# Optimization experiments

Measured on AMD Instinct MI355X. Metric: run time of the kernel, lower is better.

The kernel has to match this reference:

```python
import jax, jax.numpy as jnp
import numpy as np

B, C, D, H, W, K = 2, 192, 48, 48, 48, 7
EPS_LN = 1e-6
EPS_GRN = 1e-6


def setup_inputs() -> dict:
    key = jax.random.key(0)
    ks = jax.random.split(key, 8)
    sc = 0.02
    return {
        "x": jax.random.normal(ks[0], (B, C, D, H, W), jnp.float32),
        # depthwise conv kernel in DHWIO layout: [K,K,K,1,C] (torch weight [C,1,K,K,K])
        "conv_w": jax.random.normal(ks[1], (K, K, K, 1, C), jnp.float32) * sc,
        "conv_b": jnp.zeros((C,), jnp.float32),
        "ln_g": jnp.ones((C,), jnp.float32),
        "ln_b": jnp.zeros((C,), jnp.float32),
        "w1": jax.random.normal(ks[2], (C, 4 * C), jnp.float32) * sc,
        "b1": jnp.zeros((4 * C,), jnp.float32),
        "grn_gamma": jax.random.normal(ks[3], (4 * C,), jnp.float32) * sc,
        "grn_beta": jax.random.normal(ks[4], (4 * C,), jnp.float32) * sc,
        "w2": jax.random.normal(ks[5], (4 * C, C), jnp.float32) * sc,
        "b2": jnp.zeros((C,), jnp.float32),
    }


def reference(x, conv_w, conv_b, ln_g, ln_b, w1, b1, grn_gamma, grn_beta, w2, b2):
    c = x.shape[1]
    # NCDHW -> NDHWC (channels-last, as Permute([0,2,3,4,1]) after the conv)
    xc = jnp.transpose(x, (0, 2, 3, 4, 1))
    # depthwise conv3d, kernel 7, pad 3 (SAME for stride 1)
    y = jax.lax.conv_general_dilated(
        xc, conv_w, window_strides=(1, 1, 1), padding="SAME",
        dimension_numbers=("NDHWC", "DHWIO", "NDHWC"),
        feature_group_count=c,
    ) + conv_b
    # LayerNorm over channel dim, eps=1e-6 (biased variance, like torch)
    mu = jnp.mean(y, axis=-1, keepdims=True)
    var = jnp.mean(jnp.square(y - mu), axis=-1, keepdims=True)
    y = (y - mu) * jax.lax.rsqrt(var + EPS_LN) * ln_g + ln_b
    # MLP up + exact GELU
    y = jax.nn.gelu(y @ w1 + b1, approximate=False)
    # GRN: global L2 over spatial dims per channel
    gx = jnp.sqrt(jnp.sum(y * y, axis=(1, 2, 3), keepdims=True))  # [B,1,1,1,4C]
    nx = gx / (jnp.mean(gx, axis=-1, keepdims=True) + EPS_GRN)
    y = grn_gamma * (y * nx) + grn_beta + y
    # MLP down, permute back, residual
    y = y @ w2 + b2
    return jnp.transpose(y, (0, 4, 1, 2, 3)) + x
```

## Files before the change

kernel.cpp:

```cpp
#include <hip/hip_runtime.h>
#include <math.h>

#define Bn 2
#define Cn 192
#define Dn 48
#define Hn 48
#define Wn 48
#define C4 768
#define DHW (Dn*Hn*Wn)
#define CDHW ((long)Cn*DHW)

typedef __attribute__((ext_vector_type(8))) short bf16x8;
typedef __attribute__((ext_vector_type(4))) float f32x4;

__device__ inline float bf2f(unsigned short u) {
    union { float f; unsigned int i; } v; v.i = ((unsigned int)u) << 16; return v.f;
}
__device__ inline unsigned short f2bf(float f) {
    union { float f; unsigned int i; } v; v.f = f;
    unsigned int r = v.i + 0x7FFFu + ((v.i >> 16) & 1u);
    return (unsigned short)(r >> 16);
}
__device__ inline float blo(unsigned int u) {
    union { unsigned int i; float f; } v; v.i = u << 16; return v.f;
}
__device__ inline float bhi(unsigned int u) {
    union { unsigned int i; float f; } v; v.i = u & 0xffff0000u; return v.f;
}
__device__ inline unsigned int cvtpk_bf16(float lo, float hi) {
    unsigned int r;
    asm("v_cvt_pk_bf16_f32 %0, %1, %2" : "=v"(r) : "v"(lo), "v"(hi));
    return r;
}

__global__ __launch_bounds__(256)
void btoep_k(const float* __restrict__ cw, unsigned short* __restrict__ btp)
{
    int idx = blockIdx.x * 256 + threadIdx.x;
    int lane = idx & 63;
    int t = idx >> 6;
    int kdkh = t % 49, c = t / 49;
    int n = lane & 15, g = lane >> 4;
    unsigned short v[8];
#pragma unroll
    for (int j = 0; j < 8; ++j) {
        int kw = 8 * g + j - n;
        v[j] = (kw >= 0 && kw <= 6) ? f2bf(cw[(kdkh * 7 + kw) * Cn + c])
                                    : (unsigned short)0;
    }
    *(uint4*)(btp + (size_t)idx * 8) = *(uint4*)v;
}

#define TD 8
#define TH 16
#define TW 16
#define HD (TD+6)
#define HH (TH+6)

__global__ __launch_bounds__(128)
void conv_dw(const float* __restrict__ x, const unsigned short* __restrict__ btp,
             const float* __restrict__ cb, unsigned short* __restrict__ yc)
{
    __shared__ unsigned int xt[HD * HH * 16];
    int c = blockIdx.y;
    int s = blockIdx.x;
    int wt = s % 3, ht = (s / 3) % 3, dt = s / 9;
    int d0 = dt * TD, h0 = ht * TH, w0 = wt * TW;
    int tid = threadIdx.x;

    const float* xb = x + (long)c * DHW;
    for (int u = tid; u < HD * HH * 16; u += 128) {
        int pr = u & 15, row = u >> 4;
        int hh2 = row % HH, dd = row / HH;
        int gd = d0 - 3 + dd, gh = h0 - 3 + hh2;
        int gw0 = w0 - 3 + pr * 2;
        bool okp = (unsigned)gd < 48u && (unsigned)gh < 48u;
        const float* xr = xb + (gd * 48 + gh) * 48;
        float v0 = (okp && (unsigned)gw0 < 48u) ? xr[gw0] : 0.0f;
        float v1 = (okp && (unsigned)(gw0 + 1) < 48u) ? xr[gw0 + 1] : 0.0f;
        xt[(row << 4) + ((((pr >> 2) ^ (row & 3)) << 2) | (pr & 3))] = cvtpk_bf16(v0, v1);
    }
    __syncthreads();

    int lane = tid & 63, wv = tid >> 6;
    int lr = lane & 15, g = lane >> 4;
    float bias = cb[c];
    f32x4 acc[4];
#pragma unroll
    for (int t = 0; t < 4; ++t) acc[t] = (f32x4){bias, bias, bias, bias};

    const unsigned short* bchan = btp + (size_t)c * 49 * 512;
    const unsigned short* xt16 = (const unsigned short*)xt;

    for (int kh = 0; kh < 7; ++kh) {
        bf16x8 Bf[7];
#pragma unroll
        for (int kd = 0; kd < 7; ++kd)
            Bf[kd] = *(const bf16x8*)(bchan + (size_t)((kd * 7 + kh) * 64 + lane) * 8);
        bf16x8 Af[10];
#pragma unroll
        for (int p = 0; p < 10; ++p) {
            int r = (4 * wv + p) * HH + kh + lr;
            Af[p] = *(const bf16x8*)(xt16 + (r << 5) + ((g ^ (r & 3)) << 3));
        }
#pragma unroll
        for (int kd = 0; kd < 7; ++kd)
#pragma unroll
            for (int t = 0; t < 4; ++t)
                acc[t] = __builtin_amdgcn_mfma_f32_16x16x32_bf16(
                    Af[kd + t], Bf[kd], acc[t], 0, 0, 0);
    }

    unsigned short* yb = yc + (long)c * DHW;
#pragma unroll
    for (int t = 0; t < 4; ++t) {
        int d = d0 + 4 * wv + t;
#pragma unroll
        for (int i = 0; i < 4; ++i) {
            int h = h0 + g * 4 + i;
            yb[((long)d * 48 + h) * 48 + w0 + lr] = f2bf(acc[t][i]);
        }
    }
}

__global__ __launch_bounds__(256)
void ln_kernel(const unsigned short* __restrict__ yc, const float* __restrict__ g,
               const float* __restrict__ lb, unsigned short* __restrict__ y1)
{
    __shared__ float tile[Cn * Wn];
    __shared__ float qs1[4][48], qs2[4][48];
    __shared__ float mu_s[Wn], rs_s[Wn];
    int dh = blockIdx.x;
    long rowbase = (long)dh * Wn;
    for (int l = threadIdx.x; l < Cn * 24; l += 256) {
        int c = l / 24, wp = l % 24;
        unsigned int u = *(const unsigned int*)&yc[rowbase + (long)c * DHW + wp * 2];
        tile[c * Wn + wp * 2]     = blo(u);
        tile[c * Wn + wp * 2 + 1] = bhi(u);
    }
    __syncthreads();
    if (threadIdx.x < 192) {
        int w = threadIdx.x >> 2, q = threadIdx.x & 3;
        float s1 = 0.f, s2 = 0.f;
        for (int cc = 0; cc < 48; ++cc) {
            float v = tile[(cc * 4 + q) * Wn + w];
            s1 += v; s2 = fmaf(v, v, s2);
        }
        qs1[q][w] = s1; qs2[q][w] = s2;
    }
    __syncthreads();
    if (threadIdx.x < 48) {
        int w = threadIdx.x;
        float s1 = qs1[0][w] + qs1[1][w] + qs1[2][w] + qs1[3][w];
        float s2 = qs2[0][w] + qs2[1][w] + qs2[2][w] + qs2[3][w];
        float mu = s1 * (1.0f / Cn);
        float var = s2 * (1.0f / Cn) - mu * mu;
        mu_s[w] = mu;
        rs_s[w] = rsqrtf(var + 1e-6f);
    }
    __syncthreads();
    long obase = (long)dh * Wn * Cn;
    for (int l = threadIdx.x; l < Cn * Wn; l += 256) {
        int w = l / Cn, c = l % Cn;
        float val = (tile[c * Wn + w] - mu_s[w]) * rs_s[w] * g[c] + lb[c];
        y1[obase + l] = f2bf(val);
    }
}

__global__ __launch_bounds__(256)
void wtrans(const float* __restrict__ W, unsigned short* __restrict__ Wt, int K, int N)
{
    int idx = blockIdx.x * 256 + threadIdx.x;
    if (idx >= K * N) return;
    int n = idx / K, k = idx % K;
    Wt[idx] = f2bf(W[(long)k * N + n]);
}

__global__ __launch_bounds__(256)
void wscale(const float* __restrict__ W2, const float* __restrict__ gx2,
            const float* __restrict__ gamma, unsigned short* __restrict__ W2s)
{
    __shared__ float red[256];
    int t = threadIdx.x;
    float s = 0.f;
#pragma unroll
    for (int i = 0; i < 3; ++i) s += sqrtf(gx2[t + i * 256]);
    red[t] = s; __syncthreads();
    for (int st = 128; st > 0; st >>= 1) {
        if (t < st) red[t] += red[t + st];
        __syncthreads();
    }
    float inv = 1.0f / (red[0] * (1.0f / C4) + 1e-6f);
    int idx = blockIdx.x * 256 + t;
    int n = idx / C4, k = idx % C4;
    float snx = 1.0f + gamma[k] * sqrtf(gx2[k]) * inv;
    W2s[idx] = f2bf(W2[(long)k * Cn + n] * snx);
}

#define BM 128
#define BN 64
#define BK 64

#define GEMM_STAGE(Aptr, Astride, Btptr, Bstride)                               \
    {                                                                           \
        _Pragma("unroll")                                                       \
        for (int i = 0; i < 4; ++i) {                                           \
            int chunk = i * 256 + tid;                                          \
            int r = chunk >> 3, cc = chunk & 7;                                 \
            bf16x8 v = *(const bf16x8*)((Aptr) + (size_t)(m0 + r) * (Astride) + k0 + cc * 8); \
            *(bf16x8*)&Asm[r * BK + ((cc ^ (r & 7)) * 8)] = v;                  \
        }                                                                       \
        _Pragma("unroll")                                                       \
        for (int i = 0; i < 2; ++i) {                                           \
            int chunk = i * 256 + tid;                                          \
            int r = chunk >> 3, cc = chunk & 7;                                 \
            bf16x8 v = *(const bf16x8*)((Btptr) + (size_t)(n0 + r) * (Bstride) + k0 + cc * 8); \
            *(bf16x8*)&Bsm[r * BK + ((cc ^ (r & 7)) * 8)] = v;                  \
        }                                                                       \
    }

#define GEMM_COMPUTE                                                            \
    _Pragma("unroll")                                                           \
    for (int kk = 0; kk < 2; ++kk) {                                            \
        bf16x8 af[4], bfr[2];                                                   \
        _Pragma("unroll")                                                       \
        for (int mi = 0; mi < 4; ++mi) {                                        \
            int r = wm * 64 + mi * 16 + lr;                                     \
            int cc = (kk * 4 + lq) ^ (r & 7);                                   \
            af[mi] = *(const bf16x8*)&Asm[r * BK + cc * 8];                     \
        }                                                                       \
        _Pragma("unroll")                                                       \
        for (int ni = 0; ni < 2; ++ni) {                                        \
            int r = wn * 32 + ni * 16 + lr;                                     \
            int cc = (kk * 4 + lq) ^ (r & 7);                                   \
            bfr[ni] = *(const bf16x8*)&Bsm[r * BK + cc * 8];                    \
        }                                                                       \
        _Pragma("unroll")                                                       \
        for (int mi = 0; mi < 4; ++mi)                                          \
            _Pragma("unroll")                                                   \
            for (int ni = 0; ni < 2; ++ni)                                      \
                acc[mi][ni] = __builtin_amdgcn_mfma_f32_16x16x32_bf16(          \
                    af[mi], bfr[ni], acc[mi][ni], 0, 0, 0);                     \
    }

__global__ __launch_bounds__(256)
void gemm_up(const unsigned short* __restrict__ A, const unsigned short* __restrict__ Bt,
             const float* __restrict__ bias, unsigned short* __restrict__ Y2,
             float* __restrict__ partial)
{
    __shared__ short Asm[BM * BK];
    __shared__ short Bsm[BN * BK];
    __shared__ float colred[BN];
    int tid = threadIdx.x;
    int lane = tid & 63, wv = tid >> 6;
    int wm = wv >> 1, wn = wv & 1;
    int lr = lane & 15, lq = lane >> 4;
    long m0 = (long)blockIdx.y * BM;
    int n0 = blockIdx.x * BN;

    f32x4 acc[4][2];
#pragma unroll
    for (int mi = 0; mi < 4; ++mi)
#pragma unroll
        for (int ni = 0; ni < 2; ++ni) acc[mi][ni] = (f32x4){0.f, 0.f, 0.f, 0.f};

    for (int k0 = 0; k0 < Cn; k0 += BK) {
        GEMM_STAGE(A, Cn, Bt, Cn);
        __syncthreads();
        GEMM_COMPUTE;
        __syncthreads();
    }

    float ss[2] = {0.f, 0.f};
#pragma unroll
    for (int mi = 0; mi < 4; ++mi) {
#pragma unroll
        for (int ni = 0; ni < 2; ++ni) {
            int colg = n0 + wn * 32 + ni * 16 + lr;
            float bb = bias[colg];
            long mbase = m0 + wm * 64 + mi * 16 + lq * 4;
#pragma unroll
            for (int i = 0; i < 4; ++i) {
                float v = acc[mi][ni][i] + bb;
                v = 0.5f * v * (1.0f + erff(v * 0.70710678118654752f));
                ss[ni] = fmaf(v, v, ss[ni]);
                Y2[(mbase + i) * C4 + colg] = f2bf(v);
            }
        }
    }
#pragma unroll
    for (int ni = 0; ni < 2; ++ni) {
        ss[ni] += __shfl_xor(ss[ni], 16);
        ss[ni] += __shfl_xor(ss[ni], 32);
    }
    if (wm == 0 && lq == 0) {
        colred[wn * 32 + lr]      = ss[0];
        colred[wn * 32 + 16 + lr] = ss[1];
    }
    __syncthreads();
    if (wm == 1 && lq == 0) {
        colred[wn * 32 + lr]      += ss[0];
        colred[wn * 32 + 16 + lr] += ss[1];
    }
    __syncthreads();
    if (tid < BN) partial[(size_t)blockIdx.y * C4 + n0 + tid] = colred[tid];
}

__global__ __launch_bounds__(256)
void gemm_down(const unsigned short* __restrict__ A, const unsigned short* __restrict__ Bt,
               const float* __restrict__ beff, const float* __restrict__ x,
               float* __restrict__ out)
{
    __shared__ short Asm[BM * BK];
    __shared__ short Bsm[BN * BK];
    int tid = threadIdx.x;
    int lane = tid & 63, wv = tid >> 6;
    int wm = wv >> 1, wn = wv & 1;
    int lr = lane & 15, lq = lane >> 4;
    long m0 = (long)blockIdx.y * BM;
    int n0 = blockIdx.x * BN;

    f32x4 acc[4][2];
#pragma unroll
    for (int mi = 0; mi < 4; ++mi)
#pragma unroll
        for (int ni = 0; ni < 2; ++ni) acc[mi][ni] = (f32x4){0.f, 0.f, 0.f, 0.f};

    for (int k0 = 0; k0 < C4; k0 += BK) {
        GEMM_STAGE(A, C4, Bt, C4);
        __syncthreads();
        GEMM_COMPUTE;
        __syncthreads();
    }

#pragma unroll
    for (int mi = 0; mi < 4; ++mi) {
#pragma unroll
        for (int ni = 0; ni < 2; ++ni) {
            int colg = n0 + wn * 32 + ni * 16 + lr;
            float be = beff[colg];
            long mbase = m0 + wm * 64 + mi * 16 + lq * 4;
            const float* xp = x + (long)colg * DHW + mbase;
            float* op = out + (long)colg * DHW + mbase;
            float4 xvv = *(const float4*)xp;
            float4 o;
            o.x = acc[mi][ni][0] + be + xvv.x;
            o.y = acc[mi][ni][1] + be + xvv.y;
            o.z = acc[mi][ni][2] + be + xvv.z;
            o.w = acc[mi][ni][3] + be + xvv.w;
            *(float4*)op = o;
        }
    }
}

__global__ __launch_bounds__(256)
void grn_reduce(const float* __restrict__ partial, float* __restrict__ gx2)
{
    int n = blockIdx.x;
    const float* p = partial + n;
    float s = 0.f;
    for (int r = threadIdx.x; r < 864; r += 256) s += p[(long)r * C4];
    __shared__ float red[256];
    red[threadIdx.x] = s; __syncthreads();
    for (int st = 128; st > 0; st >>= 1) {
        if (threadIdx.x < st) red[threadIdx.x] += red[threadIdx.x + st];
        __syncthreads();
    }
    if (threadIdx.x == 0) gx2[n] = red[0];
}

__global__ __launch_bounds__(256)
void bias_eff_k(const float* __restrict__ beta, const float* __restrict__ W2,
                const float* __restrict__ b2, float* __restrict__ beff)
{
    __shared__ float red[256];
    int j = blockIdx.x, t = threadIdx.x;
    float s = 0.f;
#pragma unroll
    for (int i = 0; i < 3; ++i) {
        int k = t + i * 256;
        s = fmaf(beta[k], W2[(long)k * Cn + j], s);
    }
    red[t] = s; __syncthreads();
    for (int st = 128; st > 0; st >>= 1) {
        if (t < st) red[t] += red[t + st];
        __syncthreads();
    }
    if (t == 0) beff[j] = red[0] + b2[j];
}

extern "C" void kernel_launch(void* const* d_in, const int* in_sizes, int n_in,
                              void* d_out, int out_size, void* d_ws, size_t ws_size,
                              hipStream_t stream) {
    const float* x      = (const float*)d_in[0];
    const float* conv_w = (const float*)d_in[1];
    const float* conv_b = (const float*)d_in[2];
    const float* ln_g   = (const float*)d_in[3];
    const float* ln_b   = (const float*)d_in[4];
    const float* w1     = (const float*)d_in[5];
    const float* b1     = (const float*)d_in[6];
    const float* gg     = (const float*)d_in[7];
    const float* gb     = (const float*)d_in[8];
    const float* w2     = (const float*)d_in[9];
    const float* b2     = (const float*)d_in[10];
    float* out = (float*)d_out;
    char* ws = (char*)d_ws;

    unsigned short* y2  = (unsigned short*)(ws);
    unsigned short* yc  = (unsigned short*)(ws);
    unsigned short* y1  = (unsigned short*)(ws + 169869312L);
    unsigned short* btp = (unsigned short*)(ws + 202702848L);
    float*     partial  = (float*)(ws + 212336640L);
    unsigned short* w1t = (unsigned short*)(ws + 214990848L);
    unsigned short* w2s = (unsigned short*)(ws + 215285760L);
    float*         gx2  = (float*)(ws + 215580672L);
    float*        beff  = (float*)(ws + 215586816L);

    bias_eff_k<<<Cn, 256, 0, stream>>>(gb, w2, b2, beff);
    wtrans<<<(Cn * C4 + 255) / 256, 256, 0, stream>>>(w1, w1t, Cn, C4);

    for (int b = 0; b < Bn; ++b) {
        const float* xb = x + (size_t)b * CDHW;
        float* outb = out + (size_t)b * CDHW;
        btoep_k<<<(Cn * 49 * 64) / 256, 256, 0, stream>>>(conv_w, btp);
        dim3 gc(54, Cn);
        conv_dw<<<gc, 128, 0, stream>>>(xb, btp, conv_b, yc);
        ln_kernel<<<Dn * Hn, 256, 0, stream>>>(yc, ln_g, ln_b, y1);
        dim3 gu(C4 / BN, DHW / BM);
        gemm_up<<<gu, 256, 0, stream>>>(y1, w1t, b1, y2, partial);
        grn_reduce<<<C4, 256, 0, stream>>>(partial, gx2);
        wscale<<<(Cn * C4) / 256, 256, 0, stream>>>(w2, gx2, gg, w2s);
        dim3 gd(Cn / BN, DHW / BM);
        gemm_down<<<gd, 256, 0, stream>>>(y2, w2s, beff, xb, outb);
    }
}
```

Measured before the change: 945.9 us.

## Pre-pad input to bf16 rows and double depth tile in depthwise conv

Adds a pre-pass that converts each input W-row to bf16 in a zero-padded 64-wide layout, so the conv kernel can stage its halo with aligned 16-byte loads and no per-element bounds checks or conversion. The conv tile depth grows from 8 to 16 and each wave accumulates 8 output slices, so every loaded A fragment feeds up to 7 MFMAs and the depth halo is amortized over more outputs. The Toeplitz weight offset is shifted to match the new padding. This costs an extra pass over the input and a second workspace buffer, more accumulator registers, and half as many conv blocks.

```diff
diff --git a/kernel.cpp b/kernel.cpp
--- a/kernel.cpp
+++ b/kernel.cpp
@@ -34,6 +34,24 @@
 }
 
 __global__ __launch_bounds__(256)
+void xpad_k(const float* __restrict__ x, unsigned short* __restrict__ xbf)
+{
+    int u = blockIdx.x * 256 + threadIdx.x;
+    int j = u & 7;
+    int row = u >> 3;
+    unsigned short* orow = xbf + ((size_t)row << 6);
+    uint4 o = {0u, 0u, 0u, 0u};
+    if (j >= 1 && j <= 6) {
+        const float* xr = x + (size_t)row * 48 + (8 * j - 8);
+        float4 a = *(const float4*)xr;
+        float4 b = *(const float4*)(xr + 4);
+        o.x = cvtpk_bf16(a.x, a.y); o.y = cvtpk_bf16(a.z, a.w);
+        o.z = cvtpk_bf16(b.x, b.y); o.w = cvtpk_bf16(b.z, b.w);
+    }
+    *(uint4*)(orow + 8 * j) = o;
+}
+
+__global__ __launch_bounds__(256)
 void btoep_k(const float* __restrict__ cw, unsigned short* __restrict__ btp)
 {
     int idx = blockIdx.x * 256 + threadIdx.x;
@@ -44,50 +62,46 @@
     unsigned short v[8];
 #pragma unroll
     for (int j = 0; j < 8; ++j) {
-        int kw = 8 * g + j - n;
+        int kw = 8 * g + j - n - 5;
         v[j] = (kw >= 0 && kw <= 6) ? f2bf(cw[(kdkh * 7 + kw) * Cn + c])
                                     : (unsigned short)0;
     }
     *(uint4*)(btp + (size_t)idx * 8) = *(uint4*)v;
 }
 
-#define TD 8
-#define TH 16
-#define TW 16
-#define HD (TD+6)
-#define HH (TH+6)
+#define CTD 16
+#define CHD (CTD+6)
+#define CHH 22
 
 __global__ __launch_bounds__(128)
-void conv_dw(const float* __restrict__ x, const unsigned short* __restrict__ btp,
+void conv_dw(const unsigned short* __restrict__ xbf, const unsigned short* __restrict__ btp,
              const float* __restrict__ cb, unsigned short* __restrict__ yc)
 {
-    __shared__ unsigned int xt[HD * HH * 16];
+    __shared__ unsigned int xt[CHD * CHH * 16];
     int c = blockIdx.y;
     int s = blockIdx.x;
     int wt = s % 3, ht = (s / 3) % 3, dt = s / 9;
-    int d0 = dt * TD, h0 = ht * TH, w0 = wt * TW;
+    int d0 = dt * 16, h0 = ht * 16, w0 = wt * 16;
     int tid = threadIdx.x;
 
-    const float* xb = x + (long)c * DHW;
-    for (int u = tid; u < HD * HH * 16; u += 128) {
-        int pr = u & 15, row = u >> 4;
-        int hh2 = row % HH, dd = row / HH;
+    const unsigned short* xc = xbf + ((size_t)c * 2304 << 6);
+    for (int u = tid; u < CHD * CHH * 4; u += 128) {
+        int g = u & 3, r2 = u >> 2;
+        int hh2 = r2 % CHH, dd = r2 / CHH;
         int gd = d0 - 3 + dd, gh = h0 - 3 + hh2;
-        int gw0 = w0 - 3 + pr * 2;
-        bool okp = (unsigned)gd < 48u && (unsigned)gh < 48u;
-        const float* xr = xb + (gd * 48 + gh) * 48;
-        float v0 = (okp && (unsigned)gw0 < 48u) ? xr[gw0] : 0.0f;
-        float v1 = (okp && (unsigned)(gw0 + 1) < 48u) ? xr[gw0 + 1] : 0.0f;
-        xt[(row << 4) + ((((pr >> 2) ^ (row & 3)) << 2) | (pr & 3))] = cvtpk_bf16(v0, v1);
+        uint4 v = {0u, 0u, 0u, 0u};
+        if ((unsigned)gd < 48u && (unsigned)gh < 48u)
+            v = *(const uint4*)(xc + (((size_t)gd * 48 + gh) << 6) + w0 + 8 * g);
+        *(uint4*)&xt[(r2 << 4) + ((g ^ (r2 & 3)) << 2)] = v;
     }
     __syncthreads();
 
     int lane = tid & 63, wv = tid >> 6;
     int lr = lane & 15, g = lane >> 4;
     float bias = cb[c];
-    f32x4 acc[4];
-#pragma unroll
-    for (int t = 0; t < 4; ++t) acc[t] = (f32x4){bias, bias, bias, bias};
+    f32x4 acc[8];
+#pragma unroll
+    for (int t = 0; t < 8; ++t) acc[t] = (f32x4){bias, bias, bias, bias};
 
     const unsigned short* bchan = btp + (size_t)c * 49 * 512;
     const unsigned short* xt16 = (const unsigned short*)xt;
@@ -97,24 +111,23 @@
 #pragma unroll
         for (int kd = 0; kd < 7; ++kd)
             Bf[kd] = *(const bf16x8*)(bchan + (size_t)((kd * 7 + kh) * 64 + lane) * 8);
-        bf16x8 Af[10];
-#pragma unroll
-        for (int p = 0; p < 10; ++p) {
-            int r = (4 * wv + p) * HH + kh + lr;
-            Af[p] = *(const bf16x8*)(xt16 + (r << 5) + ((g ^ (r & 3)) << 3));
+#pragma unroll
+        for (int p = 0; p < 14; ++p) {
+            int r2 = (8 * wv + p) * CHH + kh + lr;
+            bf16x8 Af = *(const bf16x8*)(xt16 + (r2 << 5) + ((g ^ (r2 & 3)) << 3));
+#pragma unroll
+            for (int kd = 0; kd < 7; ++kd) {
+                int t = p - kd;
+                if (t < 0 || t > 7) continue;
+                acc[t] = __builtin_amdgcn_mfma_f32_16x16x32_bf16(Af, Bf[kd], acc[t], 0, 0, 0);
+            }
         }
-#pragma unroll
-        for (int kd = 0; kd < 7; ++kd)
-#pragma unroll
-            for (int t = 0; t < 4; ++t)
-                acc[t] = __builtin_amdgcn_mfma_f32_16x16x32_bf16(
-                    Af[kd + t], Bf[kd], acc[t], 0, 0, 0);
     }
 
     unsigned short* yb = yc + (long)c * DHW;
 #pragma unroll
-    for (int t = 0; t < 4; ++t) {
-        int d = d0 + 4 * wv + t;
+    for (int t = 0; t < 8; ++t) {
+        int d = d0 + 8 * wv + t;
 #pragma unroll
         for (int i = 0; i < 4; ++i) {
             int h = h0 + g * 4 + i;
@@ -406,8 +419,9 @@
     float* out = (float*)d_out;
     char* ws = (char*)d_ws;
 
+    unsigned short* yc  = (unsigned short*)(ws);
+    unsigned short* xbf = (unsigned short*)(ws + 42467328L);
     unsigned short* y2  = (unsigned short*)(ws);
-    unsigned short* yc  = (unsigned short*)(ws);
     unsigned short* y1  = (unsigned short*)(ws + 169869312L);
     unsigned short* btp = (unsigned short*)(ws + 202702848L);
     float*     partial  = (float*)(ws + 212336640L);
@@ -422,9 +436,10 @@
     for (int b = 0; b < Bn; ++b) {
         const float* xb = x + (size_t)b * CDHW;
         float* outb = out + (size_t)b * CDHW;
+        xpad_k<<<(Cn * 2304 * 8) / 256, 256, 0, stream>>>(xb, xbf);
         btoep_k<<<(Cn * 49 * 64) / 256, 256, 0, stream>>>(conv_w, btp);
-        dim3 gc(54, Cn);
-        conv_dw<<<gc, 128, 0, stream>>>(xb, btp, conv_b, yc);
+        dim3 gc(27, Cn);
+        conv_dw<<<gc, 128, 0, stream>>>(xbf, btp, conv_b, yc);
         ln_kernel<<<Dn * Hn, 256, 0, stream>>>(yc, ln_g, ln_b, y1);
         dim3 gu(C4 / BN, DHW / BM);
         gemm_up<<<gu, 256, 0, stream>>>(y1, w1t, b1, y2, partial);
```

After: 807.8 us. -14.6%, faster.
